# Kernel optimization log

Hardware: AMD Instinct MI355X
Metric: run time of the kernel (lower is better)

Reference implementation:

```python
import jax, jax.numpy as jnp
import numpy as np

SEQ, N_NODES, N_EDGES = 64, 4096, 65536
IN_CH, HID, OUT = 128, 256, 256  # conv1: IN->2*HID, conv2: 2*HID->HID; HID==OUT required by the model


def setup_inputs() -> dict:
    key = jax.random.key(0)
    ks = jax.random.split(key, 10)
    s = 0.05
    return {
        "x": jax.random.normal(ks[0], (SEQ, N_NODES, IN_CH), jnp.float32),
        "edge_index": jax.random.randint(ks[1], (SEQ, 2, N_EDGES), 0, N_NODES),
        "W1l": jax.random.normal(ks[2], (IN_CH, 2 * HID), jnp.float32) * s,
        "b1l": jnp.zeros((2 * HID,), jnp.float32),
        "W1r": jax.random.normal(ks[3], (IN_CH, 2 * HID), jnp.float32) * s,
        "W2l": jax.random.normal(ks[4], (2 * HID, HID), jnp.float32) * s,
        "b2l": jnp.zeros((HID,), jnp.float32),
        "W2r": jax.random.normal(ks[5], (2 * HID, HID), jnp.float32) * s,
        "Wih": jax.random.normal(ks[6], (3 * OUT, HID), jnp.float32) * s,
        "Whh": jax.random.normal(ks[7], (3 * OUT, OUT), jnp.float32) * s,
        "bih": jnp.zeros((3 * OUT,), jnp.float32),
        "bhh": jnp.zeros((3 * OUT,), jnp.float32),
        "timestamp": 4,
        "n_samples": 8,
    }


def _sage(xt, src, dst, Wl, bl, Wr):
    # PyG SAGEConv: lin_l(mean-aggregated neighbor msgs) + lin_r(x); bias on lin_l only
    agg = jax.ops.segment_sum(xt[src], dst, num_segments=N_NODES)
    deg = jax.ops.segment_sum(jnp.ones((src.shape[0],), xt.dtype), dst, num_segments=N_NODES)
    agg = agg / jnp.maximum(deg, 1.0)[:, None]
    return agg @ Wl + bl + xt @ Wr


def _cpc_indices(seq_len, timestamp, n_samples):
    neg_dist = seq_len // 6
    end = seq_len - n_samples - neg_dist - timestamp + 2
    start = seq_len // 8 if seq_len // 8 < end else 0
    t_samples = np.arange(start, end)
    off = np.zeros((timestamp, n_samples), np.int32)
    for i in range(1, timestamp + 1):
        off[i - 1, 0] = i  # positive sample
        for j in range(1, n_samples):
            off[i - 1, j] = i + neg_dist + j - 1  # negatives
    return t_samples, off


def reference(x, edge_index, W1l, b1l, W1r, W2l, b2l, W2r, Wih, Whh, bih, bhh, timestamp, n_samples):
    def per_t(xt, ei):
        src, dst = ei[0], ei[1]
        h = jax.nn.relu(_sage(xt, src, dst, W1l, b1l, W1r))  # dropout(p=0.5) is identity in eval
        h = _sage(h, src, dst, W2l, b2l, W2r)
        return h.max(axis=0)  # global_max_pool over the single graph

    z = jax.vmap(per_t)(x, edge_index)  # [SEQ, HID]

    # torch GRU receives [1, t+1, H] seq-major => a single GRU-cell step per element, h0 = 0
    gi = z @ Wih.T + bih  # [SEQ, 3*OUT]
    r = jax.nn.sigmoid(gi[:, :OUT] + bhh[:OUT])
    u = jax.nn.sigmoid(gi[:, OUT:2 * OUT] + bhh[OUT:2 * OUT])
    n = jnp.tanh(gi[:, 2 * OUT:] + r * bhh[2 * OUT:])
    c = (1.0 - u) * n  # [SEQ, OUT] (Whh * h0 = 0)

    seq_len = z.shape[0]
    t_samples, off = _cpc_indices(seq_len, timestamp, n_samples)
    cnt = len(t_samples)
    idx = t_samples[:, None, None] + off[None]  # [T, timestamp, n_samples]
    enc = z[idx]  # [T, ts, ns, F]
    ct = c[t_samples]  # [T, F]

    eps = 1e-8  # torch cosine_similarity eps
    num = jnp.einsum('tijd,td->tij', enc, ct)
    den = jnp.maximum(jnp.linalg.norm(enc, axis=-1), eps) * \
          jnp.maximum(jnp.linalg.norm(ct, axis=-1), eps)[:, None, None]
    total = num / den  # [T, ts, ns]

    nce = -jax.nn.log_softmax(total, axis=-1)[..., 0].sum() / (cnt * timestamp)
    correct = (jnp.argmax(total, axis=-1) == 0).sum()  # softmax is monotone -> same argmax
    acc = correct / (cnt * timestamp)
    hidden = c[:t_samples[-1] + 1][None]  # GRU hidden of last loop iter: [1, t_last+1, OUT]
    return nce, acc, hidden
```

## Files before the change

kernel.cpp:

```cpp
#include <hip/hip_runtime.h>

#define T_SEQ 64
#define NV 4096
#define NE 65536
#define CIN 128
#define H2 512
#define HO 256
#define NEG_FLT (-3.402823466e38f)

typedef unsigned short u16;
typedef __bf16 bf16x8 __attribute__((ext_vector_type(8)));
typedef float f32x4 __attribute__((ext_vector_type(4)));

__device__ __forceinline__ u16 f2bf(float f){
  unsigned u = __float_as_uint(f);
  unsigned r = (u + 0x7FFFu + ((u >> 16) & 1u)) >> 16;
  return (u16)r;
}
__device__ __forceinline__ float bf2f(u16 h){
  return __uint_as_float(((unsigned)h) << 16);
}

__device__ __forceinline__ int swz8(){
  return (int)((blockIdx.x & 7) * (gridDim.x >> 3) + (blockIdx.x >> 3));
}

__device__ __forceinline__ void gll16(const u16* g, const uint4* l){
  __builtin_amdgcn_global_load_lds(
      reinterpret_cast<const __attribute__((address_space(1))) unsigned int*>(
          reinterpret_cast<uintptr_t>(g)),
      reinterpret_cast<__attribute__((address_space(3))) unsigned int*>(
          reinterpret_cast<uintptr_t>(l)),
      16, 0, 0);
}

struct Lay {
  size_t z, c, zn, cn, Bt1h, Bt1l, Bt2h, Bt2l, cnt, fill, rowptr, deginv, csr,
         aggh, aggl, xh, xl, hh, hl, mh, partial, total;
};
static Lay mk_layout(int tc){
  Lay L; size_t o = 0;
  auto tk = [&](size_t b){ size_t p = o; o += ((b + 255) & ~(size_t)255); return p; };
  L.z       = tk((size_t)T_SEQ * HO * 4);
  L.c       = tk((size_t)T_SEQ * HO * 4);
  L.zn      = tk((size_t)T_SEQ * 4);
  L.cn      = tk((size_t)T_SEQ * 4);
  L.Bt1h    = tk((size_t)512 * 256 * 2);
  L.Bt1l    = tk((size_t)512 * 256 * 2);
  L.Bt2h    = tk((size_t)512 * 512 * 2);
  L.Bt2l    = tk((size_t)512 * 512 * 2);
  L.cnt     = tk((size_t)tc * NV * 4);
  L.fill    = tk((size_t)tc * NV * 4);
  L.rowptr  = tk((size_t)tc * (NV + 1) * 4);
  L.deginv  = tk((size_t)tc * NV * 4);
  L.csr     = tk((size_t)tc * NE * 4);
  L.aggh    = tk((size_t)tc * NV * CIN * 2);
  L.aggl    = tk((size_t)tc * NV * CIN * 2);
  L.xh      = tk((size_t)tc * NV * CIN * 2);
  L.xl      = tk((size_t)tc * NV * CIN * 2);
  L.hh      = tk((size_t)tc * NV * H2 * 2);
  L.hl      = tk((size_t)tc * NV * H2 * 2);
  L.mh      = tk((size_t)tc * NV * H2 * 4);
  L.partial = tk((size_t)tc * 128 * HO * 4);
  L.total = o; return L;
}

__global__ void k_init_out(float* out){
  int i = threadIdx.x;
  if (i < 2) out[i] = 0.0f;
}

__global__ void k_prep_Bt(const float* __restrict__ W1l, const float* __restrict__ W1r,
                          const float* __restrict__ W2l, const float* __restrict__ W2r,
                          u16* __restrict__ Bt1h, u16* __restrict__ Bt1l,
                          u16* __restrict__ Bt2h, u16* __restrict__ Bt2l){
  int i = blockIdx.x * 256 + threadIdx.x;
  if (i < 512 * 256){
    int n = i >> 8, k = i & 255;
    float v = (k < 128) ? W1l[k * 512 + n] : W1r[(k - 128) * 512 + n];
    u16 h = f2bf(v);
    Bt1h[i] = h; Bt1l[i] = f2bf(v - bf2f(h));
  } else {
    int j = i - 512 * 256;
    if (j < 512 * 512){
      int n = j >> 9, k = j & 511;
      float v = (n < 256) ? W2l[k * 256 + n] : W2r[k * 256 + (n - 256)];
      u16 h = f2bf(v);
      Bt2h[j] = h; Bt2l[j] = f2bf(v - bf2f(h));
    }
  }
}

__global__ void k_zero(int* p, int n){
  int i = blockIdx.x * 256 + threadIdx.x;
  if (i < n) p[i] = 0;
}

__global__ void k_count(const int* __restrict__ ei, int t0, int tc, int* __restrict__ cnt){
  int i = blockIdx.x * 256 + threadIdx.x;
  if (i >= tc * NE) return;
  int tl = i >> 16, e = i & (NE - 1);
  int dst = ei[(size_t)(t0 + tl) * 2 * NE + NE + e];
  atomicAdd(&cnt[tl * NV + dst], 1);
}

__global__ void k_scan(const int* __restrict__ cnt, int* __restrict__ rowptr,
                       float* __restrict__ deginv){
  int tl = blockIdx.x, tid = threadIdx.x;
  __shared__ int s[256];
  int vals[16]; int sum = 0;
  const int* cb = cnt + tl * NV + tid * 16;
  #pragma unroll
  for (int i = 0; i < 16; i++){ vals[i] = cb[i]; sum += vals[i]; }
  s[tid] = sum; __syncthreads();
  for (int off = 1; off < 256; off <<= 1){
    int v = (tid >= off) ? s[tid - off] : 0;
    __syncthreads();
    s[tid] += v;
    __syncthreads();
  }
  int ex = s[tid] - sum;
  int* rp = rowptr + tl * (NV + 1) + tid * 16;
  float* dv = deginv + tl * NV + tid * 16;
  #pragma unroll
  for (int i = 0; i < 16; i++){
    rp[i] = ex; ex += vals[i];
    int d = vals[i] < 1 ? 1 : vals[i];
    dv[i] = 1.0f / (float)d;
  }
  if (tid == 255) rowptr[tl * (NV + 1) + NV] = ex;
}

__global__ void k_fill(const int* __restrict__ ei, int t0, int tc,
                       const int* __restrict__ rowptr, int* __restrict__ fill,
                       int* __restrict__ csr){
  int i = blockIdx.x * 256 + threadIdx.x;
  if (i >= tc * NE) return;
  int tl = i >> 16, e = i & (NE - 1);
  const int* eit = ei + (size_t)(t0 + tl) * 2 * NE;
  int src = eit[e], dst = eit[NE + e];
  int pos = atomicAdd(&fill[tl * NV + dst], 1);
  csr[tl * NE + rowptr[tl * (NV + 1) + dst] + pos] = src;
}

__global__ void k_xsplit(const float* __restrict__ xs, int n4,
                         u16* __restrict__ xh, u16* __restrict__ xl){
  int i = blockIdx.x * 256 + threadIdx.x;
  if (i >= n4) return;
  float4 v = ((const float4*)xs)[i];
  u16 h0 = f2bf(v.x), h1 = f2bf(v.y), h2 = f2bf(v.z), h3 = f2bf(v.w);
  u16 l0 = f2bf(v.x - bf2f(h0)), l1 = f2bf(v.y - bf2f(h1));
  u16 l2 = f2bf(v.z - bf2f(h2)), l3 = f2bf(v.w - bf2f(h3));
  ushort4 hv; hv.x = h0; hv.y = h1; hv.z = h2; hv.w = h3;
  ushort4 lv; lv.x = l0; lv.y = l1; lv.z = l2; lv.w = l3;
  *(ushort4*)(xh + (size_t)i * 4) = hv;
  *(ushort4*)(xl + (size_t)i * 4) = lv;
}

__global__ __launch_bounds__(256) void k_agg1(const float* __restrict__ x, int t0, int tc,
                       const int* __restrict__ rowptr, const int* __restrict__ csr,
                       const float* __restrict__ deginv,
                       u16* __restrict__ aggh, u16* __restrict__ aggl){
  int bid = swz8();
  int w = (bid * 256 + threadIdx.x) >> 6;
  int lane = threadIdx.x & 63;
  if (w >= tc * NV) return;
  int tl = w >> 12, v = w & (NV - 1);
  const float2* xt = (const float2*)(x + (size_t)(t0 + tl) * NV * CIN);
  int beg = rowptr[tl * (NV + 1) + v], end = rowptr[tl * (NV + 1) + v + 1];
  const int* cs = csr + tl * NE;
  float ax = 0.f, ay = 0.f;
  int j = beg;
  for (; j + 1 < end; j += 2){
    int s0 = cs[j], s1 = cs[j + 1];
    float2 x0 = xt[(size_t)s0 * 64 + lane];
    float2 x1 = xt[(size_t)s1 * 64 + lane];
    ax += x0.x + x1.x; ay += x0.y + x1.y;
  }
  if (j < end){
    int s0 = cs[j];
    float2 x0 = xt[(size_t)s0 * 64 + lane];
    ax += x0.x; ay += x0.y;
  }
  float di = deginv[tl * NV + v];
  float vx = ax * di, vy = ay * di;
  u16 hx = f2bf(vx), hy = f2bf(vy);
  u16 lx = f2bf(vx - bf2f(hx)), ly = f2bf(vy - bf2f(hy));
  ushort2 hv; hv.x = hx; hv.y = hy;
  ushort2 lv; lv.x = lx; lv.y = ly;
  ((ushort2*)aggh)[(size_t)w * 64 + lane] = hv;
  ((ushort2*)aggl)[(size_t)w * 64 + lane] = lv;
}

__global__ __launch_bounds__(256, 2) void k_gemm_mfma(
    const u16* __restrict__ Ah0, const u16* __restrict__ Al0,
    const u16* __restrict__ Ah1, const u16* __restrict__ Al1,
    int ksplit, int lda,
    const u16* __restrict__ Bh, const u16* __restrict__ Bl, int K,
    const float* __restrict__ bias, int mode,
    u16* __restrict__ OutH, u16* __restrict__ OutL, float* __restrict__ OutF)
{
  __shared__ uint4 lds[4096];
  int tid = threadIdx.x;
  int bid = swz8();
  int bm = bid >> 2, bn = bid & 3;
  size_t row0 = (size_t)bm * 128;
  int col0 = bn * 128;
  int lane = tid & 63, wid = tid >> 6;
  int wm = wid >> 1, wn = wid & 1;
  int l15 = lane & 15, l4 = lane >> 4;

  size_t aoff[2], boff[2];
  int cslot[2];
  #pragma unroll
  for (int q = 0; q < 2; q++){
    int c = 2 * wid + q;
    aoff[q] = (row0 + c * 16 + l15) * (size_t)lda + (size_t)(l4 * 8);
    boff[q] = (size_t)(col0 + c * 16 + l15) * K + (size_t)(l4 * 8);
    cslot[q] = c * 64;
  }

#define STAGE(T) do { \
    int kk0_ = (T) << 5; \
    const u16* pAh_ = Ah0; const u16* pAl_ = Al0; int kA_ = kk0_; \
    if (kk0_ >= ksplit){ pAh_ = Ah1; pAl_ = Al1; kA_ = kk0_ - ksplit; } \
    int bb_ = ((T) & 1) << 11; \
    _Pragma("unroll") \
    for (int q = 0; q < 2; q++){ \
      gll16(pAh_ + aoff[q] + kA_, &lds[bb_ + cslot[q]]); \
      gll16(pAl_ + aoff[q] + kA_, &lds[bb_ + 512 + cslot[q]]); \
      gll16(Bh + boff[q] + kk0_, &lds[bb_ + 1024 + cslot[q]]); \
      gll16(Bl + boff[q] + kk0_, &lds[bb_ + 1536 + cslot[q]]); \
    } \
  } while (0)

  f32x4 zv = {0.f, 0.f, 0.f, 0.f};
  f32x4 acc[4][4];
  #pragma unroll
  for (int i = 0; i < 4; i++)
    #pragma unroll
    for (int j = 0; j < 4; j++) acc[i][j] = zv;

  STAGE(0);
  __syncthreads();

  int nt = K >> 5;
  for (int t = 0; t < nt; t++){
    if (t + 1 < nt) STAGE(t + 1);
    int base = (t & 1) << 11;
    int abase = base + wm * 256;
    int bbase = base + 1024 + wn * 256;
    bf16x8 ah[4], al[4], bh[4], bl[4];
    #pragma unroll
    for (int f = 0; f < 4; f++){
      ah[f] = __builtin_bit_cast(bf16x8, lds[abase + f * 64 + lane]);
      al[f] = __builtin_bit_cast(bf16x8, lds[abase + 512 + f * 64 + lane]);
      bh[f] = __builtin_bit_cast(bf16x8, lds[bbase + f * 64 + lane]);
      bl[f] = __builtin_bit_cast(bf16x8, lds[bbase + 512 + f * 64 + lane]);
    }
    #pragma unroll
    for (int i = 0; i < 4; i++)
      #pragma unroll
      for (int j = 0; j < 4; j++){
        acc[i][j] = __builtin_amdgcn_mfma_f32_16x16x32_bf16(ah[i], bh[j], acc[i][j], 0, 0, 0);
        acc[i][j] = __builtin_amdgcn_mfma_f32_16x16x32_bf16(ah[i], bl[j], acc[i][j], 0, 0, 0);
        acc[i][j] = __builtin_amdgcn_mfma_f32_16x16x32_bf16(al[i], bh[j], acc[i][j], 0, 0, 0);
      }
    __syncthreads();
  }
#undef STAGE

  #pragma unroll
  for (int i = 0; i < 4; i++){
    #pragma unroll
    for (int j = 0; j < 4; j++){
      int col = col0 + wn * 64 + j * 16 + l15;
      float bv = bias ? bias[col] : 0.f;
      #pragma unroll
      for (int r = 0; r < 4; r++){
        size_t row = row0 + wm * 64 + i * 16 + l4 * 4 + r;
        float v = acc[i][j][r] + bv;
        if (mode == 1){
          v = fmaxf(v, 0.f);
          u16 h = f2bf(v);
          u16 l = f2bf(v - bf2f(h));
          OutH[row * 512 + col] = h;
          OutL[row * 512 + col] = l;
        } else {
          OutF[row * 512 + col] = v;
        }
      }
    }
  }
}

__global__ __launch_bounds__(256) void k_conv2agg(
    const float* __restrict__ mh, const int* __restrict__ rowptr,
    const int* __restrict__ csr, const float* __restrict__ deginv,
    const float* __restrict__ b2l, float* __restrict__ partial){
  int blk = swz8();
  int tl = blk >> 7, nb = blk & 127;
  int wid = threadIdx.x >> 6, lane = threadIdx.x & 63;
  const float4* m4 = (const float4*)mh;
  const int* rp = rowptr + tl * (NV + 1);
  const int* cs = csr + tl * NE;
  size_t tB = (size_t)tl * NV;
  float4 bb = ((const float4*)b2l)[lane];
  float4 vmax; vmax.x = NEG_FLT; vmax.y = NEG_FLT; vmax.z = NEG_FLT; vmax.w = NEG_FLT;
  int v0 = nb * 32 + wid * 8;
  for (int q = 0; q < 8; q++){
    int v = v0 + q;
    int beg = rp[v], end = rp[v + 1];
    float4 acc; acc.x = 0.f; acc.y = 0.f; acc.z = 0.f; acc.w = 0.f;
    int j = beg;
    for (; j + 1 < end; j += 2){
      int s0 = cs[j], s1 = cs[j + 1];
      float4 a0 = m4[(tB + s0) * 128 + lane];
      float4 a1 = m4[(tB + s1) * 128 + lane];
      acc.x += a0.x + a1.x; acc.y += a0.y + a1.y;
      acc.z += a0.z + a1.z; acc.w += a0.w + a1.w;
    }
    if (j < end){
      int s0 = cs[j];
      float4 a0 = m4[(tB + s0) * 128 + lane];
      acc.x += a0.x; acc.y += a0.y; acc.z += a0.z; acc.w += a0.w;
    }
    float di = deginv[tl * NV + v];
    float4 hr = m4[(tB + v) * 128 + 64 + lane];
    float4 val;
    val.x = acc.x * di + bb.x + hr.x;
    val.y = acc.y * di + bb.y + hr.y;
    val.z = acc.z * di + bb.z + hr.z;
    val.w = acc.w * di + bb.w + hr.w;
    vmax.x = fmaxf(vmax.x, val.x); vmax.y = fmaxf(vmax.y, val.y);
    vmax.z = fmaxf(vmax.z, val.z); vmax.w = fmaxf(vmax.w, val.w);
  }
  __shared__ float4 sm[4][64];
  sm[wid][lane] = vmax;
  __syncthreads();
  if (wid == 0){
    float4 a = sm[0][lane], b = sm[1][lane], c = sm[2][lane], d = sm[3][lane];
    float4 r;
    r.x = fmaxf(fmaxf(a.x, b.x), fmaxf(c.x, d.x));
    r.y = fmaxf(fmaxf(a.y, b.y), fmaxf(c.y, d.y));
    r.z = fmaxf(fmaxf(a.z, b.z), fmaxf(c.z, d.z));
    r.w = fmaxf(fmaxf(a.w, b.w), fmaxf(c.w, d.w));
    ((float4*)partial)[((size_t)(tl * 128 + nb)) * 64 + lane] = r;
  }
}

__global__ void k_pool(const float* __restrict__ partial, int t0, int tc,
                       float* __restrict__ z, float* __restrict__ zn){
  int tl = blockIdx.x, c = threadIdx.x;
  float m = NEG_FLT;
  for (int b = 0; b < 128; b++)
    m = fmaxf(m, partial[((size_t)(tl * 128 + b)) * HO + c]);
  z[(t0 + tl) * HO + c] = m;
  __shared__ float s[256];
  s[c] = m * m; __syncthreads();
  for (int off = 128; off > 0; off >>= 1){
    if (c < off) s[c] += s[c + off];
    __syncthreads();
  }
  if (c == 0) zn[t0 + tl] = sqrtf(s[0]);
}

__global__ void k_gru(const float* __restrict__ z, const float* __restrict__ Wih,
                      const float* __restrict__ bih, const float* __restrict__ bhh,
                      float* __restrict__ c, float* __restrict__ cn, float* __restrict__ out){
  int s0 = blockIdx.x, j = threadIdx.x;
  __shared__ float zs[256];
  __shared__ float ss[256];
  zs[j] = z[s0 * HO + j];
  __syncthreads();
  const float* wr = Wih + (size_t)j * HO;
  const float* wu = Wih + (size_t)(HO + j) * HO;
  const float* wn = Wih + (size_t)(2 * HO + j) * HO;
  float gr = bih[j], gu = bih[HO + j], gn = bih[2 * HO + j];
  for (int k = 0; k < HO; k++){
    float zv = zs[k];
    gr = fmaf(zv, wr[k], gr);
    gu = fmaf(zv, wu[k], gu);
    gn = fmaf(zv, wn[k], gn);
  }
  float r = 1.f / (1.f + expf(-(gr + bhh[j])));
  float u = 1.f / (1.f + expf(-(gu + bhh[HO + j])));
  float n = tanhf(gn + r * bhh[2 * HO + j]);
  float cv = (1.f - u) * n;
  c[s0 * HO + j] = cv;
  if (s0 < 44) out[2 + s0 * HO + j] = cv;
  ss[j] = cv * cv; __syncthreads();
  for (int off = 128; off > 0; off >>= 1){
    if (j < off) ss[j] += ss[j + off];
    __syncthreads();
  }
  if (j == 0) cn[s0] = sqrtf(ss[0]);
}

__global__ void k_cpc(const float* __restrict__ z, const float* __restrict__ c,
                      const float* __restrict__ zn, const float* __restrict__ cn,
                      float* __restrict__ out){
  int tt = blockIdx.x;
  int ts = 8 + tt;
  int tid = threadIdx.x;
  __shared__ float ct[256];
  __shared__ float tot[32];
  ct[tid] = c[ts * HO + tid];
  __syncthreads();
  int g = tid >> 3, r = tid & 7;
  int i = g >> 3, j = g & 7;
  int idx = ts + ((j == 0) ? (i + 1) : (i + j + 10));
  const float* zr = z + idx * HO;
  float s = 0.f;
  for (int k = r; k < HO; k += 8) s = fmaf(zr[k], ct[k], s);
  s += __shfl_down(s, 4, 8);
  s += __shfl_down(s, 2, 8);
  s += __shfl_down(s, 1, 8);
  if (r == 0){
    float den = fmaxf(zn[idx], 1e-8f) * fmaxf(cn[ts], 1e-8f);
    tot[g] = s / den;
  }
  __syncthreads();
  if (tid < 4){
    const float* tr = tot + tid * 8;
    float m = tr[0];
    for (int q = 1; q < 8; q++) m = fmaxf(m, tr[q]);
    float se = 0.f;
    for (int q = 0; q < 8; q++) se += expf(tr[q] - m);
    float lse = m + logf(se);
    float nce = (lse - tr[0]) * (1.0f / 144.0f);
    float corr = (tr[0] == m) ? (1.0f / 144.0f) : 0.f;
    atomicAdd(&out[0], nce);
    atomicAdd(&out[1], corr);
  }
}

extern "C" void kernel_launch(void* const* d_in, const int* in_sizes, int n_in,
                              void* d_out, int out_size, void* d_ws, size_t ws_size,
                              hipStream_t stream){
  const float* x   = (const float*)d_in[0];
  const int*   ei  = (const int*)  d_in[1];
  const float* W1l = (const float*)d_in[2];
  const float* b1l = (const float*)d_in[3];
  const float* W1r = (const float*)d_in[4];
  const float* W2l = (const float*)d_in[5];
  const float* b2l = (const float*)d_in[6];
  const float* W2r = (const float*)d_in[7];
  const float* Wih = (const float*)d_in[8];
  const float* bih = (const float*)d_in[10];
  const float* bhh = (const float*)d_in[11];
  float* out = (float*)d_out;

  int tc = 64;
  while (tc > 1 && mk_layout(tc).total > ws_size) tc >>= 1;
  Lay L = mk_layout(tc);
  char* w = (char*)d_ws;
  float* zB   = (float*)(w + L.z);
  float* cB   = (float*)(w + L.c);
  float* znB  = (float*)(w + L.zn);
  float* cnB  = (float*)(w + L.cn);
  u16*   Bt1h = (u16*)  (w + L.Bt1h);
  u16*   Bt1l = (u16*)  (w + L.Bt1l);
  u16*   Bt2h = (u16*)  (w + L.Bt2h);
  u16*   Bt2l = (u16*)  (w + L.Bt2l);
  int*   cnt  = (int*)  (w + L.cnt);
  int*   fill = (int*)  (w + L.fill);
  int*   rp   = (int*)  (w + L.rowptr);
  float* dinv = (float*)(w + L.deginv);
  int*   csr  = (int*)  (w + L.csr);
  u16*   aggh = (u16*)  (w + L.aggh);
  u16*   aggl = (u16*)  (w + L.aggl);
  u16*   xh   = (u16*)  (w + L.xh);
  u16*   xl   = (u16*)  (w + L.xl);
  u16*   hh   = (u16*)  (w + L.hh);
  u16*   hl   = (u16*)  (w + L.hl);
  float* mhB  = (float*)(w + L.mh);
  float* part = (float*)(w + L.partial);

  hipLaunchKernelGGL(k_init_out, dim3(1), dim3(64), 0, stream, out);
  hipLaunchKernelGGL(k_prep_Bt, dim3(1536), dim3(256), 0, stream,
                     W1l, W1r, W2l, W2r, Bt1h, Bt1l, Bt2h, Bt2l);

  for (int t0 = 0; t0 < T_SEQ; t0 += tc){
    int nE = tc * NE;
    int M = tc * NV;
    hipLaunchKernelGGL(k_zero, dim3((tc * NV + 255) / 256), dim3(256), 0, stream, cnt, tc * NV);
    hipLaunchKernelGGL(k_zero, dim3((tc * NV + 255) / 256), dim3(256), 0, stream, fill, tc * NV);
    hipLaunchKernelGGL(k_count, dim3((nE + 255) / 256), dim3(256), 0, stream, ei, t0, tc, cnt);
    hipLaunchKernelGGL(k_scan, dim3(tc), dim3(256), 0, stream, cnt, rp, dinv);
    hipLaunchKernelGGL(k_fill, dim3((nE + 255) / 256), dim3(256), 0, stream, ei, t0, tc, rp, fill, csr);
    hipLaunchKernelGGL(k_agg1, dim3(tc * NV / 4), dim3(256), 0, stream,
                       x, t0, tc, rp, csr, dinv, aggh, aggl);
    int n4 = tc * NV * CIN / 4;
    hipLaunchKernelGGL(k_xsplit, dim3((n4 + 255) / 256), dim3(256), 0, stream,
                       x + (size_t)t0 * NV * CIN, n4, xh, xl);
    hipLaunchKernelGGL(k_gemm_mfma, dim3((M / 128) * 4), dim3(256), 0, stream,
                       aggh, aggl, xh, xl, 128, CIN,
                       Bt1h, Bt1l, 256, b1l, 1, hh, hl, (float*)nullptr);
    hipLaunchKernelGGL(k_gemm_mfma, dim3((M / 128) * 4), dim3(256), 0, stream,
                       hh, hl, hh, hl, 1 << 30, H2,
                       Bt2h, Bt2l, 512, (const float*)nullptr, 0,
                       (u16*)nullptr, (u16*)nullptr, mhB);
    hipLaunchKernelGGL(k_conv2agg, dim3(tc * 128), dim3(256), 0, stream,
                       mhB, rp, csr, dinv, b2l, part);
    hipLaunchKernelGGL(k_pool, dim3(tc), dim3(256), 0, stream, part, t0, tc, zB, znB);
  }

  hipLaunchKernelGGL(k_gru, dim3(T_SEQ), dim3(256), 0, stream, zB, Wih, bih, bhh, cB, cnB, out);
  hipLaunchKernelGGL(k_cpc, dim3(36), dim3(256), 0, stream, zB, cB, znB, cnB, out);
  (void)in_sizes; (void)n_in; (void)out_size;
}
```

Before: 2.433 ms.

## Fuse x bf16 split into agg1, merge zero kernels, refine GEMM sync and pooling

Folds the x hi/lo bf16 split into the neighbour aggregation kernel, so x is read once per node there and a separate pass over x is removed. The two zeroing launches become one kernel. The GEMM loop replaces __syncthreads with an explicit vmcnt wait plus a raw barrier, so the next stage's loads can stay in flight while the current tile is computed. The pool kernel is spread across four times as many blocks, and the z-row norms move into the CPC kernel. The hand-written waitcnt counts are fragile and could break correctness if the load count per stage ever changes.

```diff
diff --git a/kernel.cpp b/kernel.cpp
--- a/kernel.cpp
+++ b/kernel.cpp
@@ -33,6 +33,11 @@
           reinterpret_cast<uintptr_t>(l)),
       16, 0, 0);
 }
+
+#define WAITV(N) asm volatile("s_waitcnt vmcnt(" #N ")" ::: "memory")
+#define BARRIER() do{ asm volatile("" ::: "memory"); \
+                      __builtin_amdgcn_s_barrier(); \
+                      asm volatile("" ::: "memory"); }while(0)
 
 struct Lay {
   size_t z, c, zn, cn, Bt1h, Bt1l, Bt2h, Bt2l, cnt, fill, rowptr, deginv, csr,
@@ -91,9 +96,9 @@
   }
 }
 
-__global__ void k_zero(int* p, int n){
+__global__ void k_zero2(int* __restrict__ p, int* __restrict__ q, int n){
   int i = blockIdx.x * 256 + threadIdx.x;
-  if (i < n) p[i] = 0;
+  if (i < n){ p[i] = 0; q[i] = 0; }
 }
 
 __global__ void k_count(const int* __restrict__ ei, int t0, int tc, int* __restrict__ cnt){
@@ -143,24 +148,11 @@
   csr[tl * NE + rowptr[tl * (NV + 1) + dst] + pos] = src;
 }
 
-__global__ void k_xsplit(const float* __restrict__ xs, int n4,
-                         u16* __restrict__ xh, u16* __restrict__ xl){
-  int i = blockIdx.x * 256 + threadIdx.x;
-  if (i >= n4) return;
-  float4 v = ((const float4*)xs)[i];
-  u16 h0 = f2bf(v.x), h1 = f2bf(v.y), h2 = f2bf(v.z), h3 = f2bf(v.w);
-  u16 l0 = f2bf(v.x - bf2f(h0)), l1 = f2bf(v.y - bf2f(h1));
-  u16 l2 = f2bf(v.z - bf2f(h2)), l3 = f2bf(v.w - bf2f(h3));
-  ushort4 hv; hv.x = h0; hv.y = h1; hv.z = h2; hv.w = h3;
-  ushort4 lv; lv.x = l0; lv.y = l1; lv.z = l2; lv.w = l3;
-  *(ushort4*)(xh + (size_t)i * 4) = hv;
-  *(ushort4*)(xl + (size_t)i * 4) = lv;
-}
-
 __global__ __launch_bounds__(256) void k_agg1(const float* __restrict__ x, int t0, int tc,
                        const int* __restrict__ rowptr, const int* __restrict__ csr,
                        const float* __restrict__ deginv,
-                       u16* __restrict__ aggh, u16* __restrict__ aggl){
+                       u16* __restrict__ aggh, u16* __restrict__ aggl,
+                       u16* __restrict__ xh, u16* __restrict__ xl){
   int bid = swz8();
   int w = (bid * 256 + threadIdx.x) >> 6;
   int lane = threadIdx.x & 63;
@@ -190,6 +182,13 @@
   ushort2 lv; lv.x = lx; lv.y = ly;
   ((ushort2*)aggh)[(size_t)w * 64 + lane] = hv;
   ((ushort2*)aggl)[(size_t)w * 64 + lane] = lv;
+  float2 xv = xt[(size_t)v * 64 + lane];
+  u16 xhx = f2bf(xv.x), xhy = f2bf(xv.y);
+  u16 xlx = f2bf(xv.x - bf2f(xhx)), xly = f2bf(xv.y - bf2f(xhy));
+  ushort2 av; av.x = xhx; av.y = xhy;
+  ushort2 bv; bv.x = xlx; bv.y = xly;
+  ((ushort2*)xh)[(size_t)w * 64 + lane] = av;
+  ((ushort2*)xl)[(size_t)w * 64 + lane] = bv;
 }
 
 __global__ __launch_bounds__(256, 2) void k_gemm_mfma(
@@ -242,11 +241,12 @@
     for (int j = 0; j < 4; j++) acc[i][j] = zv;
 
   STAGE(0);
-  __syncthreads();
 
   int nt = K >> 5;
   for (int t = 0; t < nt; t++){
-    if (t + 1 < nt) STAGE(t + 1);
+    if (t + 1 < nt){ STAGE(t + 1); WAITV(8); }
+    else          { WAITV(0); }
+    BARRIER();
     int base = (t & 1) << 11;
     int abase = base + wm * 256;
     int bbase = base + 1024 + wn * 256;
@@ -266,7 +266,7 @@
         acc[i][j] = __builtin_amdgcn_mfma_f32_16x16x32_bf16(ah[i], bl[j], acc[i][j], 0, 0, 0);
         acc[i][j] = __builtin_amdgcn_mfma_f32_16x16x32_bf16(al[i], bh[j], acc[i][j], 0, 0, 0);
       }
-    __syncthreads();
+    BARRIER();
   }
 #undef STAGE
 
@@ -349,20 +349,23 @@
   }
 }
 
-__global__ void k_pool(const float* __restrict__ partial, int t0, int tc,
-                       float* __restrict__ z, float* __restrict__ zn){
-  int tl = blockIdx.x, c = threadIdx.x;
+__global__ void k_pool(const float* __restrict__ partial, int t0,
+                       float* __restrict__ z){
+  int blk = blockIdx.x;
+  int tl = blk >> 2, cg = blk & 3;
+  int tid = threadIdx.x;
+  int c = cg * 64 + (tid & 63);
+  int grp = tid >> 6;
   float m = NEG_FLT;
-  for (int b = 0; b < 128; b++)
+  for (int b = grp; b < 128; b += 4)
     m = fmaxf(m, partial[((size_t)(tl * 128 + b)) * HO + c]);
-  z[(t0 + tl) * HO + c] = m;
-  __shared__ float s[256];
-  s[c] = m * m; __syncthreads();
-  for (int off = 128; off > 0; off >>= 1){
-    if (c < off) s[c] += s[c + off];
-    __syncthreads();
-  }
-  if (c == 0) zn[t0 + tl] = sqrtf(s[0]);
+  __shared__ float s[4][64];
+  s[grp][tid & 63] = m;
+  __syncthreads();
+  if (grp == 0){
+    m = fmaxf(fmaxf(s[0][tid], s[1][tid]), fmaxf(s[2][tid], s[3][tid]));
+    z[(t0 + tl) * HO + c] = m;
+  }
 }
 
 __global__ void k_gru(const float* __restrict__ z, const float* __restrict__ Wih,
@@ -398,8 +401,7 @@
 }
 
 __global__ void k_cpc(const float* __restrict__ z, const float* __restrict__ c,
-                      const float* __restrict__ zn, const float* __restrict__ cn,
-                      float* __restrict__ out){
+                      const float* __restrict__ cn, float* __restrict__ out){
   int tt = blockIdx.x;
   int ts = 8 + tt;
   int tid = threadIdx.x;
@@ -411,13 +413,17 @@
   int i = g >> 3, j = g & 7;
   int idx = ts + ((j == 0) ? (i + 1) : (i + j + 10));
   const float* zr = z + idx * HO;
-  float s = 0.f;
-  for (int k = r; k < HO; k += 8) s = fmaf(zr[k], ct[k], s);
-  s += __shfl_down(s, 4, 8);
-  s += __shfl_down(s, 2, 8);
-  s += __shfl_down(s, 1, 8);
+  float s = 0.f, nz = 0.f;
+  for (int k = r; k < HO; k += 8){
+    float zv = zr[k];
+    s = fmaf(zv, ct[k], s);
+    nz = fmaf(zv, zv, nz);
+  }
+  s += __shfl_down(s, 4, 8);  nz += __shfl_down(nz, 4, 8);
+  s += __shfl_down(s, 2, 8);  nz += __shfl_down(nz, 2, 8);
+  s += __shfl_down(s, 1, 8);  nz += __shfl_down(nz, 1, 8);
   if (r == 0){
-    float den = fmaxf(zn[idx], 1e-8f) * fmaxf(cn[ts], 1e-8f);
+    float den = fmaxf(sqrtf(nz), 1e-8f) * fmaxf(cn[ts], 1e-8f);
     tot[g] = s / den;
   }
   __syncthreads();
@@ -457,7 +463,6 @@
   char* w = (char*)d_ws;
   float* zB   = (float*)(w + L.z);
   float* cB   = (float*)(w + L.c);
-  float* znB  = (float*)(w + L.zn);
   float* cnB  = (float*)(w + L.cn);
   u16*   Bt1h = (u16*)  (w + L.Bt1h);
   u16*   Bt1l = (u16*)  (w + L.Bt1l);
@@ -484,16 +489,13 @@
   for (int t0 = 0; t0 < T_SEQ; t0 += tc){
     int nE = tc * NE;
     int M = tc * NV;
-    hipLaunchKernelGGL(k_zero, dim3((tc * NV + 255) / 256), dim3(256), 0, stream, cnt, tc * NV);
-    hipLaunchKernelGGL(k_zero, dim3((tc * NV + 255) / 256), dim3(256), 0, stream, fill, tc * NV);
+    hipLaunchKernelGGL(k_zero2, dim3((tc * NV + 255) / 256), dim3(256), 0, stream,
+                       cnt, fill, tc * NV);
     hipLaunchKernelGGL(k_count, dim3((nE + 255) / 256), dim3(256), 0, stream, ei, t0, tc, cnt);
     hipLaunchKernelGGL(k_scan, dim3(tc), dim3(256), 0, stream, cnt, rp, dinv);
     hipLaunchKernelGGL(k_fill, dim3((nE + 255) / 256), dim3(256), 0, stream, ei, t0, tc, rp, fill, csr);
     hipLaunchKernelGGL(k_agg1, dim3(tc * NV / 4), dim3(256), 0, stream,
-                       x, t0, tc, rp, csr, dinv, aggh, aggl);
-    int n4 = tc * NV * CIN / 4;
-    hipLaunchKernelGGL(k_xsplit, dim3((n4 + 255) / 256), dim3(256), 0, stream,
-                       x + (size_t)t0 * NV * CIN, n4, xh, xl);
+                       x, t0, tc, rp, csr, dinv, aggh, aggl, xh, xl);
     hipLaunchKernelGGL(k_gemm_mfma, dim3((M / 128) * 4), dim3(256), 0, stream,
                        aggh, aggl, xh, xl, 128, CIN,
                        Bt1h, Bt1l, 256, b1l, 1, hh, hl, (float*)nullptr);
@@ -503,10 +505,10 @@
                        (u16*)nullptr, (u16*)nullptr, mhB);
     hipLaunchKernelGGL(k_conv2agg, dim3(tc * 128), dim3(256), 0, stream,
                        mhB, rp, csr, dinv, b2l, part);
-    hipLaunchKernelGGL(k_pool, dim3(tc), dim3(256), 0, stream, part, t0, tc, zB, znB);
+    hipLaunchKernelGGL(k_pool, dim3(tc * 4), dim3(256), 0, stream, part, t0, zB);
   }
 
   hipLaunchKernelGGL(k_gru, dim3(T_SEQ), dim3(256), 0, stream, zB, Wih, bih, bhh, cB, cnB, out);
-  hipLaunchKernelGGL(k_cpc, dim3(36), dim3(256), 0, stream, zB, cB, znB, cnB, out);
+  hipLaunchKernelGGL(k_cpc, dim3(36), dim3(256), 0, stream, zB, cB, cnB, out);
   (void)in_sizes; (void)n_in; (void)out_size;
 }
```

Measured after the change: 2.301 ms. 1.06x faster.
